# Kernel tuning notes

Hardware: AMD Instinct MI355X
Metric: run time of the kernel (lower is better)

Reference implementation:

```python
import jax, jax.numpy as jnp
import numpy as np

B, T, WARM, H, FIN, MLPW = 8192, 30, 24, 128, 8, 128
WX = ['clouds','pres','precip','temp','rh','ghi','wind_x','wind_y']
TL = ['hour_sin','hour_cos','year_sin','year_cos','elev_angle','azimuth_sin','azimuth_cos']


def setup_inputs() -> dict:
    key = jax.random.key(0)
    ks = jax.random.split(key, 32)
    d = {}
    for i, n in enumerate(WX + TL):
        d[n] = jax.random.normal(ks[i], (B, T), dtype=jnp.float32)
    d['irradiance_in'] = jax.random.uniform(ks[20], (B, WARM), dtype=jnp.float32)
    s = lambda fan: 1.0 / np.sqrt(fan).astype(np.float32)
    # LSTM params (flax OptimizedLSTMCell math: fused input/hidden kernels, one bias), gate order i,f,g,o
    d['Wi'] = jax.random.normal(ks[21], (FIN, 4 * H), dtype=jnp.float32) * s(FIN)
    d['Wh'] = jax.random.normal(ks[22], (H, 4 * H), dtype=jnp.float32) * s(H)
    d['b'] = jnp.zeros((4 * H,), jnp.float32)
    # output head: MLP(depth=2, width=128) with relu, then Dense(1)
    d['W1'] = jax.random.normal(ks[23], (H, MLPW), dtype=jnp.float32) * s(H)
    d['b1'] = jnp.zeros((MLPW,), jnp.float32)
    d['W2'] = jax.random.normal(ks[24], (MLPW, MLPW), dtype=jnp.float32) * s(MLPW)
    d['b2'] = jnp.zeros((MLPW,), jnp.float32)
    d['Wout'] = jax.random.normal(ks[25], (MLPW, 1), dtype=jnp.float32) * s(MLPW)
    d['bout'] = jnp.zeros((1,), jnp.float32)
    return d


def reference(clouds, pres, precip, temp, rh, ghi, wind_x, wind_y,
              hour_sin, hour_cos, year_sin, year_cos, elev_angle, azimuth_sin, azimuth_cos,
              irradiance_in, Wi, Wh, b, W1, b1, W2, b2, Wout, bout):
    # FLAGS.weather=False path: x is the time/location feature stack [B, T, 7].
    # Weather features are accepted (as in the original dict) but unused.
    x = jnp.stack([hour_sin, hour_cos, year_sin, year_cos, elev_angle, azimuth_sin, azimuth_cos], axis=-1)
    warm_in = jnp.concatenate([x[:, :WARM], irradiance_in[..., None]], axis=-1)  # [B, 24, 8]
    auto_in = x[:, WARM:]                                                        # [B, 6, 7]

    def lstm_step(c, h, inp):
        z = inp @ Wi + h @ Wh + b                    # [B, 4H]
        i, f, g, o = jnp.split(z, 4, axis=-1)
        c2 = jax.nn.sigmoid(f) * c + jax.nn.sigmoid(i) * jnp.tanh(g)
        h2 = jax.nn.sigmoid(o) * jnp.tanh(c2)
        return c2, h2

    def out_mlp(h):
        h = jax.nn.relu(h @ W1 + b1)
        h = jax.nn.relu(h @ W2 + b2)
        return h @ Wout + bout                       # [..., 1]

    c0 = jnp.zeros((x.shape[0], H), x.dtype)
    h0 = jnp.zeros((x.shape[0], H), x.dtype)

    # warmup: teacher-forced LSTM over observed irradiance
    def warm_step(carry, xt):
        c, h = carry
        c, h = lstm_step(c, h, xt)
        return (c, h), h
    (c, h), hs = jax.lax.scan(warm_step, (c0, h0), jnp.swapaxes(warm_in, 0, 1))
    preds_warm = out_mlp(jnp.swapaxes(hs, 0, 1))     # [B, 24, 1]
    last_pred = preds_warm[:, -1]                    # [B, 1]

    def auto_step(carry, xt):
        c, h, p = carry
        c, h = lstm_step(c, h, jnp.concatenate([xt, p], axis=-1))
        p = out_mlp(h)
        return (c, h, p), p
    _, preds_auto = jax.lax.scan(auto_step, (c, h, last_pred), jnp.swapaxes(auto_in, 0, 1))
    preds_auto = jnp.swapaxes(preds_auto, 0, 1)      # [B, 6, 1]

    pred = jnp.concatenate([preds_warm, preds_auto], axis=1)  # [B, 30, 1]
    return jnp.squeeze(pred, axis=2)                 # [B, 30]
```

## Files before the change

### kernel.cpp

```cpp
#include <hip/hip_runtime.h>


#define T_STEPS 30
#define WARM_N  24

typedef __attribute__((ext_vector_type(8)))  short short8;
typedef __attribute__((ext_vector_type(4)))  float float4v;

struct FeatPtrs { const float* f[7]; };

__device__ __forceinline__ short f2bf(float f){
  unsigned u = __float_as_uint(f);
  unsigned r = (u + 0x7fffu + ((u >> 16) & 1u)) >> 16;
  return (short)r;
}
__device__ __forceinline__ float bf2f(short h){
  return __uint_as_float(((unsigned)(unsigned short)h) << 16);
}

#if __has_builtin(__builtin_amdgcn_rcpf)
#define RCP(x) __builtin_amdgcn_rcpf(x)
#else
#define RCP(x) (1.0f/(x))
#endif

__device__ __forceinline__ float sigm(float x){ return RCP(1.0f + __expf(-x)); }
__device__ __forceinline__ float tanh_(float x){ return 1.0f - 2.0f*RCP(1.0f + __expf(2.0f*x)); }

__global__ void pack_weights(const float* __restrict__ Wi, const float* __restrict__ Wh,
                             const float* __restrict__ W1, const float* __restrict__ W2,
                             short* __restrict__ ws)
{
  int idx = blockIdx.x * 256 + threadIdx.x;
  if (idx >= 224 * 512) return;
  int f    = idx >> 9;
  int r    = idx & 511;
  int lane = r >> 3, j = r & 7;
  int kk   = ((lane >> 4) << 3) + j;
  int c16  = lane & 15;
  float v = 0.0f;
  if (f < 160){
    int wt = f / 20, rem = f % 20, g = rem / 5, ks = rem % 5;
    int col = g * 128 + wt * 16 + c16;
    if (ks == 0){
      if (kk < 8)        v = Wi[kk * 512 + col];
      else if (kk < 16)  v = Wi[(kk - 8) * 512 + col];
      else               v = 0.0f;
    } else {
      v = Wh[((ks - 1) * 32 + kk) * 512 + col];
    }
  } else {
    int f2 = f - 160;
    const float* W = (f2 < 32) ? W1 : W2;
    int f3 = f2 & 31;
    int wt = f3 >> 2, ks = f3 & 3;
    v = W[(ks * 32 + kk) * 128 + wt * 16 + c16];
  }
  ws[idx] = f2bf(v);
}

__global__ __launch_bounds__(512, 2)
void lstm_mfma(FeatPtrs fp, const float* __restrict__ irr,
               const short* __restrict__ wsb,
               const float* __restrict__ bz, const float* __restrict__ b1,
               const float* __restrict__ b2, const float* __restrict__ Wout,
               const float* __restrict__ bout, float* __restrict__ out)
{
  __shared__ __align__(16) short xp[2][1280];
  __shared__ __align__(16) short hhi[4 * 1280];
  __shared__ __align__(16) short hlo[4 * 1280];
  __shared__ __align__(16) short o1p[4 * 1280];
  __shared__ __align__(16) float o2s[32 * 132];
  __shared__ float WoutS[128];
  __shared__ float pS[32];

  const int t   = threadIdx.x;
  const int l   = t & 63;
  const int w   = t >> 6;
  const int c16 = l & 15;
  const int kq  = l >> 4;
  const int r0  = blockIdx.x * 32;

  short8 Bz[4][5], B1f[4], B2f[4];
  {
    const short8* f8 = (const short8*)wsb;
#pragma unroll
    for (int g = 0; g < 4; ++g)
#pragma unroll
      for (int ks = 0; ks < 5; ++ks)
        Bz[g][ks] = f8[((w * 4 + g) * 5 + ks) * 64 + l];
#pragma unroll
    for (int ks = 0; ks < 4; ++ks) B1f[ks] = f8[(160 + w * 4 + ks) * 64 + l];
#pragma unroll
    for (int ks = 0; ks < 4; ++ks) B2f[ks] = f8[(192 + w * 4 + ks) * 64 + l];
  }
  float bzv[4];
#pragma unroll
  for (int g = 0; g < 4; ++g) bzv[g] = bz[g * 128 + w * 16 + c16];
  const float b1v   = b1[w * 16 + c16];
  const float b2v   = b2[w * 16 + c16];
  const float bout0 = bout[0];
  if (t < 128) WoutS[t] = Wout[t];

  {
    int* p = (int*)xp;
    for (int i = t; i < 1280; i += 512) p[i] = 0;
    p = (int*)hhi;
    for (int i = t; i < 2560; i += 512) p[i] = 0;
    p = (int*)hlo;
    for (int i = t; i < 2560; i += 512) p[i] = 0;
  }

  float cst[8];
#pragma unroll
  for (int i = 0; i < 8; ++i) cst[i] = 0.0f;

  const int aoff = c16 * 40 + kq * 8;
  const int wb   = (w >> 1) * 1280 + (w & 1) * 16 + c16;
  __syncthreads();

  if (t < 256){
    int r = t >> 3, j = t & 7;
    float v = (j < 7) ? fp.f[j][(r0 + r) * T_STEPS] : irr[(r0 + r) * WARM_N];
    int base = (r >> 4) * 640 + (r & 15) * 40 + j;
    short hi = f2bf(v);
    xp[0][base] = hi;
    xp[0][base + 8] = f2bf(v - bf2f(hi));
  }
  __syncthreads();

  for (int i = 0; i < 23; ++i){
    if (t < 256){
      int r = t >> 3, j = t & 7;
      float v = (j < 7) ? fp.f[j][(r0 + r) * T_STEPS + (i + 1)]
                        : irr[(r0 + r) * WARM_N + (i + 1)];
      int base = (r >> 4) * 640 + (r & 15) * 40 + j;
      short hi = f2bf(v);
      short* xb = xp[(i + 1) & 1];
      xb[base] = hi;
      xb[base + 8] = f2bf(v - bf2f(hi));
    }
    float4v acc[4][2];
#pragma unroll
    for (int g = 0; g < 4; ++g)
#pragma unroll
      for (int m = 0; m < 2; ++m)
#pragma unroll
        for (int r = 0; r < 4; ++r) acc[g][m][r] = bzv[g];
    float4v m1[2];
#pragma unroll
    for (int m = 0; m < 2; ++m)
#pragma unroll
      for (int r = 0; r < 4; ++r) m1[m][r] = b1v;
    {
      const short* xb = xp[i & 1];
      short8 a0 = *(const short8*)&xb[aoff];
      short8 a1 = *(const short8*)&xb[640 + aoff];
#pragma unroll
      for (int g = 0; g < 4; ++g){
        acc[g][0] = __builtin_amdgcn_mfma_f32_16x16x32_bf16(a0, Bz[g][0], acc[g][0], 0, 0, 0);
        acc[g][1] = __builtin_amdgcn_mfma_f32_16x16x32_bf16(a1, Bz[g][0], acc[g][1], 0, 0, 0);
      }
    }
#pragma unroll
    for (int ks = 0; ks < 4; ++ks){
      short8 ah0 = *(const short8*)&hhi[ks * 1280 + aoff];
      short8 al0 = *(const short8*)&hlo[ks * 1280 + aoff];
      short8 ah1 = *(const short8*)&hhi[ks * 1280 + 640 + aoff];
      short8 al1 = *(const short8*)&hlo[ks * 1280 + 640 + aoff];
#pragma unroll
      for (int g = 0; g < 4; ++g){
        acc[g][0] = __builtin_amdgcn_mfma_f32_16x16x32_bf16(ah0, Bz[g][1 + ks], acc[g][0], 0, 0, 0);
        acc[g][0] = __builtin_amdgcn_mfma_f32_16x16x32_bf16(al0, Bz[g][1 + ks], acc[g][0], 0, 0, 0);
        acc[g][1] = __builtin_amdgcn_mfma_f32_16x16x32_bf16(ah1, Bz[g][1 + ks], acc[g][1], 0, 0, 0);
        acc[g][1] = __builtin_amdgcn_mfma_f32_16x16x32_bf16(al1, Bz[g][1 + ks], acc[g][1], 0, 0, 0);
      }
      if (i >= 1){
        m1[0] = __builtin_amdgcn_mfma_f32_16x16x32_bf16(ah0, B1f[ks], m1[0], 0, 0, 0);
        m1[0] = __builtin_amdgcn_mfma_f32_16x16x32_bf16(al0, B1f[ks], m1[0], 0, 0, 0);
        m1[1] = __builtin_amdgcn_mfma_f32_16x16x32_bf16(ah1, B1f[ks], m1[1], 0, 0, 0);
        m1[1] = __builtin_amdgcn_mfma_f32_16x16x32_bf16(al1, B1f[ks], m1[1], 0, 0, 0);
      }
    }
    if (i >= 1){
#pragma unroll
      for (int m = 0; m < 2; ++m)
#pragma unroll
        for (int r = 0; r < 4; ++r)
          o1p[wb + m * 640 + (kq * 4 + r) * 40] = f2bf(fmaxf(m1[m][r], 0.0f));
    }
    if (i >= 2 && t < 256){
      int r = t >> 3, jj = t & 7;
      const float* orow = &o2s[r * 132 + jj * 16];
      const float* wrow = &WoutS[jj * 16];
      float s = 0.0f;
#pragma unroll
      for (int q = 0; q < 16; ++q) s += orow[q] * wrow[q];
      s += __shfl_down(s, 4, 8);
      s += __shfl_down(s, 2, 8);
      s += __shfl_down(s, 1, 8);
      if (jj == 0){
        float pv = s + bout0;
        out[(r0 + r) * T_STEPS + (i - 2)] = pv;
        pS[r] = pv;
      }
    }
    __syncthreads();

#pragma unroll
    for (int m = 0; m < 2; ++m)
#pragma unroll
      for (int r = 0; r < 4; ++r){
        float zi = acc[0][m][r], zf = acc[1][m][r], zg = acc[2][m][r], zo = acc[3][m][r];
        float c2 = sigm(zf) * cst[m * 4 + r] + sigm(zi) * tanh_(zg);
        cst[m * 4 + r] = c2;
        float h2 = sigm(zo) * tanh_(c2);
        int addr = wb + m * 640 + (kq * 4 + r) * 40;
        short hi = f2bf(h2);
        hhi[addr] = hi;
        hlo[addr] = f2bf(h2 - bf2f(hi));
      }
    if (i >= 1){
      float4v m2[2];
#pragma unroll
      for (int m = 0; m < 2; ++m)
#pragma unroll
        for (int r = 0; r < 4; ++r) m2[m][r] = b2v;
#pragma unroll
      for (int ks = 0; ks < 4; ++ks){
#pragma unroll
        for (int m = 0; m < 2; ++m){
          short8 a = *(const short8*)&o1p[ks * 1280 + m * 640 + aoff];
          m2[m] = __builtin_amdgcn_mfma_f32_16x16x32_bf16(a, B2f[ks], m2[m], 0, 0, 0);
        }
      }
#pragma unroll
      for (int m = 0; m < 2; ++m)
#pragma unroll
        for (int r = 0; r < 4; ++r)
          o2s[(m * 16 + kq * 4 + r) * 132 + w * 16 + c16] = fmaxf(m2[m][r], 0.0f);
    }
    __syncthreads();
  }

  {
    float4v m1[2];
#pragma unroll
    for (int m = 0; m < 2; ++m)
#pragma unroll
      for (int r = 0; r < 4; ++r) m1[m][r] = b1v;
#pragma unroll
    for (int ks = 0; ks < 4; ++ks){
      short8 ah0 = *(const short8*)&hhi[ks * 1280 + aoff];
      short8 al0 = *(const short8*)&hlo[ks * 1280 + aoff];
      short8 ah1 = *(const short8*)&hhi[ks * 1280 + 640 + aoff];
      short8 al1 = *(const short8*)&hlo[ks * 1280 + 640 + aoff];
      m1[0] = __builtin_amdgcn_mfma_f32_16x16x32_bf16(ah0, B1f[ks], m1[0], 0, 0, 0);
      m1[0] = __builtin_amdgcn_mfma_f32_16x16x32_bf16(al0, B1f[ks], m1[0], 0, 0, 0);
      m1[1] = __builtin_amdgcn_mfma_f32_16x16x32_bf16(ah1, B1f[ks], m1[1], 0, 0, 0);
      m1[1] = __builtin_amdgcn_mfma_f32_16x16x32_bf16(al1, B1f[ks], m1[1], 0, 0, 0);
    }
#pragma unroll
    for (int m = 0; m < 2; ++m)
#pragma unroll
      for (int r = 0; r < 4; ++r)
        o1p[wb + m * 640 + (kq * 4 + r) * 40] = f2bf(fmaxf(m1[m][r], 0.0f));
    if (t < 256){
      int r = t >> 3, jj = t & 7;
      const float* orow = &o2s[r * 132 + jj * 16];
      const float* wrow = &WoutS[jj * 16];
      float s = 0.0f;
#pragma unroll
      for (int q = 0; q < 16; ++q) s += orow[q] * wrow[q];
      s += __shfl_down(s, 4, 8);
      s += __shfl_down(s, 2, 8);
      s += __shfl_down(s, 1, 8);
      if (jj == 0){
        float pv = s + bout0;
        out[(r0 + r) * T_STEPS + 21] = pv;
        pS[r] = pv;
      }
    }
    __syncthreads();
    float4v m2[2];
#pragma unroll
    for (int m = 0; m < 2; ++m)
#pragma unroll
      for (int r = 0; r < 4; ++r) m2[m][r] = b2v;
#pragma unroll
    for (int ks = 0; ks < 4; ++ks){
#pragma unroll
      for (int m = 0; m < 2; ++m){
        short8 a = *(const short8*)&o1p[ks * 1280 + m * 640 + aoff];
        m2[m] = __builtin_amdgcn_mfma_f32_16x16x32_bf16(a, B2f[ks], m2[m], 0, 0, 0);
      }
    }
#pragma unroll
    for (int m = 0; m < 2; ++m)
#pragma unroll
      for (int r = 0; r < 4; ++r)
        o2s[(m * 16 + kq * 4 + r) * 132 + w * 16 + c16] = fmaxf(m2[m][r], 0.0f);
    __syncthreads();
    if (t < 256){
      int r = t >> 3, jj = t & 7;
      const float* orow = &o2s[r * 132 + jj * 16];
      const float* wrow = &WoutS[jj * 16];
      float s = 0.0f;
#pragma unroll
      for (int q = 0; q < 16; ++q) s += orow[q] * wrow[q];
      s += __shfl_down(s, 4, 8);
      s += __shfl_down(s, 2, 8);
      s += __shfl_down(s, 1, 8);
      if (jj == 0){
        float pv = s + bout0;
        out[(r0 + r) * T_STEPS + 22] = pv;
        pS[r] = pv;
      }
    }
    __syncthreads();
  }

  for (int s = 23; s < T_STEPS; ++s){
    if (s > 23){
      if (t < 256){
        int r = t >> 3, j = t & 7;
        float v = (j < 7) ? fp.f[j][(r0 + r) * T_STEPS + s] : pS[r];
        int base = (r >> 4) * 640 + (r & 15) * 40 + j;
        short hi = f2bf(v);
        short* xb = xp[s & 1];
        xb[base] = hi;
        xb[base + 8] = f2bf(v - bf2f(hi));
      }
      __syncthreads();
    }
    float4v acc[4][2];
#pragma unroll
    for (int g = 0; g < 4; ++g)
#pragma unroll
      for (int m = 0; m < 2; ++m)
#pragma unroll
        for (int r = 0; r < 4; ++r) acc[g][m][r] = bzv[g];
    {
      const short* xb = xp[s & 1];
      short8 a0 = *(const short8*)&xb[aoff];
      short8 a1 = *(const short8*)&xb[640 + aoff];
#pragma unroll
      for (int g = 0; g < 4; ++g){
        acc[g][0] = __builtin_amdgcn_mfma_f32_16x16x32_bf16(a0, Bz[g][0], acc[g][0], 0, 0, 0);
        acc[g][1] = __builtin_amdgcn_mfma_f32_16x16x32_bf16(a1, Bz[g][0], acc[g][1], 0, 0, 0);
      }
    }
#pragma unroll
    for (int ks = 0; ks < 4; ++ks){
      short8 ah0 = *(const short8*)&hhi[ks * 1280 + aoff];
      short8 al0 = *(const short8*)&hlo[ks * 1280 + aoff];
      short8 ah1 = *(const short8*)&hhi[ks * 1280 + 640 + aoff];
      short8 al1 = *(const short8*)&hlo[ks * 1280 + 640 + aoff];
#pragma unroll
      for (int g = 0; g < 4; ++g){
        acc[g][0] = __builtin_amdgcn_mfma_f32_16x16x32_bf16(ah0, Bz[g][1 + ks], acc[g][0], 0, 0, 0);
        acc[g][0] = __builtin_amdgcn_mfma_f32_16x16x32_bf16(al0, Bz[g][1 + ks], acc[g][0], 0, 0, 0);
        acc[g][1] = __builtin_amdgcn_mfma_f32_16x16x32_bf16(ah1, Bz[g][1 + ks], acc[g][1], 0, 0, 0);
        acc[g][1] = __builtin_amdgcn_mfma_f32_16x16x32_bf16(al1, Bz[g][1 + ks], acc[g][1], 0, 0, 0);
      }
    }
    __syncthreads();
#pragma unroll
    for (int m = 0; m < 2; ++m)
#pragma unroll
      for (int r = 0; r < 4; ++r){
        float zi = acc[0][m][r], zf = acc[1][m][r], zg = acc[2][m][r], zo = acc[3][m][r];
        float c2 = sigm(zf) * cst[m * 4 + r] + sigm(zi) * tanh_(zg);
        cst[m * 4 + r] = c2;
        float h2 = sigm(zo) * tanh_(c2);
        int addr = wb + m * 640 + (kq * 4 + r) * 40;
        short hi = f2bf(h2);
        hhi[addr] = hi;
        hlo[addr] = f2bf(h2 - bf2f(hi));
      }
    __syncthreads();
    float4v m1[2];
#pragma unroll
    for (int m = 0; m < 2; ++m)
#pragma unroll
      for (int r = 0; r < 4; ++r) m1[m][r] = b1v;
#pragma unroll
    for (int ks = 0; ks < 4; ++ks){
      short8 ah0 = *(const short8*)&hhi[ks * 1280 + aoff];
      short8 al0 = *(const short8*)&hlo[ks * 1280 + aoff];
      short8 ah1 = *(const short8*)&hhi[ks * 1280 + 640 + aoff];
      short8 al1 = *(const short8*)&hlo[ks * 1280 + 640 + aoff];
      m1[0] = __builtin_amdgcn_mfma_f32_16x16x32_bf16(ah0, B1f[ks], m1[0], 0, 0, 0);
      m1[0] = __builtin_amdgcn_mfma_f32_16x16x32_bf16(al0, B1f[ks], m1[0], 0, 0, 0);
      m1[1] = __builtin_amdgcn_mfma_f32_16x16x32_bf16(ah1, B1f[ks], m1[1], 0, 0, 0);
      m1[1] = __builtin_amdgcn_mfma_f32_16x16x32_bf16(al1, B1f[ks], m1[1], 0, 0, 0);
    }
#pragma unroll
    for (int m = 0; m < 2; ++m)
#pragma unroll
      for (int r = 0; r < 4; ++r)
        o1p[wb + m * 640 + (kq * 4 + r) * 40] = f2bf(fmaxf(m1[m][r], 0.0f));
    __syncthreads();
    float4v m2[2];
#pragma unroll
    for (int m = 0; m < 2; ++m)
#pragma unroll
      for (int r = 0; r < 4; ++r) m2[m][r] = b2v;
#pragma unroll
    for (int ks = 0; ks < 4; ++ks){
#pragma unroll
      for (int m = 0; m < 2; ++m){
        short8 a = *(const short8*)&o1p[ks * 1280 + m * 640 + aoff];
        m2[m] = __builtin_amdgcn_mfma_f32_16x16x32_bf16(a, B2f[ks], m2[m], 0, 0, 0);
      }
    }
#pragma unroll
    for (int m = 0; m < 2; ++m)
#pragma unroll
      for (int r = 0; r < 4; ++r)
        o2s[(m * 16 + kq * 4 + r) * 132 + w * 16 + c16] = fmaxf(m2[m][r], 0.0f);
    __syncthreads();
    if (t < 256){
      int r = t >> 3, jj = t & 7;
      const float* orow = &o2s[r * 132 + jj * 16];
      const float* wrow = &WoutS[jj * 16];
      float ssum = 0.0f;
#pragma unroll
      for (int q = 0; q < 16; ++q) ssum += orow[q] * wrow[q];
      ssum += __shfl_down(ssum, 4, 8);
      ssum += __shfl_down(ssum, 2, 8);
      ssum += __shfl_down(ssum, 1, 8);
      if (jj == 0){
        float pv = ssum + bout0;
        out[(r0 + r) * T_STEPS + s] = pv;
        pS[r] = pv;
      }
    }
    __syncthreads();
  }
}

extern "C" void kernel_launch(void* const* d_in, const int* in_sizes, int n_in,
                              void* d_out, int out_size, void* d_ws, size_t ws_size,
                              hipStream_t stream)
{
  (void)in_sizes; (void)n_in; (void)out_size; (void)ws_size;
  FeatPtrs fp;
  for (int j = 0; j < 7; ++j) fp.f[j] = (const float*)d_in[8 + j];
  const float* irr  = (const float*)d_in[15];
  const float* Wi   = (const float*)d_in[16];
  const float* Wh   = (const float*)d_in[17];
  const float* bz   = (const float*)d_in[18];
  const float* W1   = (const float*)d_in[19];
  const float* b1   = (const float*)d_in[20];
  const float* W2   = (const float*)d_in[21];
  const float* b2   = (const float*)d_in[22];
  const float* Wout = (const float*)d_in[23];
  const float* bout = (const float*)d_in[24];

  short* ws = (short*)d_ws;
  pack_weights<<<dim3(448), dim3(256), 0, stream>>>(Wi, Wh, W1, W2, ws);
  lstm_mfma<<<dim3(256), dim3(512), 0, stream>>>(
      fp, irr, ws, bz, b1, b2, Wout, bout, (float*)d_out);
}
```

Baseline: 205.8 us.

## Switch LSTM MFMA to fp16 single-pass and overlap autoregressive head with gate matmul

Replaces the bf16 hi/lo split (two MFMAs per product for hidden state and inputs) with a single fp16 MFMA, roughly halving the tensor-core work and LDS traffic per step. The autoregressive loop is restructured so the gate matmul for step s runs before the previous prediction is known. The fed-back prediction's contribution is then added as a rank-1 fp32 correction using cached Wi row 7, which removes one barrier-serialized stage per step. This trades accuracy, since fp16 has a narrower range and the split compensation is gone, for fewer MFMAs and shorter per-step critical paths.

```diff
diff --git a/kernel.cpp b/kernel.cpp
--- a/kernel.cpp
+++ b/kernel.cpp
@@ -4,19 +4,10 @@
 #define T_STEPS 30
 #define WARM_N  24
 
-typedef __attribute__((ext_vector_type(8)))  short short8;
-typedef __attribute__((ext_vector_type(4)))  float float4v;
+typedef _Float16 h8 __attribute__((ext_vector_type(8)));
+typedef __attribute__((ext_vector_type(4))) float float4v;
 
 struct FeatPtrs { const float* f[7]; };
-
-__device__ __forceinline__ short f2bf(float f){
-  unsigned u = __float_as_uint(f);
-  unsigned r = (u + 0x7fffu + ((u >> 16) & 1u)) >> 16;
-  return (short)r;
-}
-__device__ __forceinline__ float bf2f(short h){
-  return __uint_as_float(((unsigned)(unsigned short)h) << 16);
-}
 
 #if __has_builtin(__builtin_amdgcn_rcpf)
 #define RCP(x) __builtin_amdgcn_rcpf(x)
@@ -29,7 +20,7 @@
 
 __global__ void pack_weights(const float* __restrict__ Wi, const float* __restrict__ Wh,
                              const float* __restrict__ W1, const float* __restrict__ W2,
-                             short* __restrict__ ws)
+                             _Float16* __restrict__ ws)
 {
   int idx = blockIdx.x * 256 + threadIdx.x;
   if (idx >= 224 * 512) return;
@@ -42,13 +33,8 @@
   if (f < 160){
     int wt = f / 20, rem = f % 20, g = rem / 5, ks = rem % 5;
     int col = g * 128 + wt * 16 + c16;
-    if (ks == 0){
-      if (kk < 8)        v = Wi[kk * 512 + col];
-      else if (kk < 16)  v = Wi[(kk - 8) * 512 + col];
-      else               v = 0.0f;
-    } else {
-      v = Wh[((ks - 1) * 32 + kk) * 512 + col];
-    }
+    if (ks == 0) v = (kk < 8) ? Wi[kk * 512 + col] : 0.0f;
+    else         v = Wh[((ks - 1) * 32 + kk) * 512 + col];
   } else {
     int f2 = f - 160;
     const float* W = (f2 < 32) ? W1 : W2;
@@ -56,20 +42,43 @@
     int wt = f3 >> 2, ks = f3 & 3;
     v = W[(ks * 32 + kk) * 128 + wt * 16 + c16];
   }
-  ws[idx] = f2bf(v);
+  ws[idx] = (_Float16)v;
 }
+
+__device__ __forceinline__ void head_do(int t, int r0, int step,
+    const float* o2s, const float* WoutS, float bout0,
+    float* __restrict__ out, float* pS)
+{
+  if (t < 256){
+    int r = t >> 3, jj = t & 7;
+    const float* orow = &o2s[r * 132 + jj * 16];
+    const float* wrow = &WoutS[jj * 16];
+    float s = 0.0f;
+#pragma unroll
+    for (int q = 0; q < 16; ++q) s += orow[q] * wrow[q];
+    s += __shfl_down(s, 4, 8);
+    s += __shfl_down(s, 2, 8);
+    s += __shfl_down(s, 1, 8);
+    if (jj == 0){
+      float pv = s + bout0;
+      out[(r0 + r) * T_STEPS + step] = pv;
+      pS[r] = pv;
+    }
+  }
+}
+
+#define MFMA16 __builtin_amdgcn_mfma_f32_16x16x32_f16
 
 __global__ __launch_bounds__(512, 2)
 void lstm_mfma(FeatPtrs fp, const float* __restrict__ irr,
-               const short* __restrict__ wsb,
+               const _Float16* __restrict__ wsb,
                const float* __restrict__ bz, const float* __restrict__ b1,
                const float* __restrict__ b2, const float* __restrict__ Wout,
                const float* __restrict__ bout, float* __restrict__ out)
 {
-  __shared__ __align__(16) short xp[2][1280];
-  __shared__ __align__(16) short hhi[4 * 1280];
-  __shared__ __align__(16) short hlo[4 * 1280];
-  __shared__ __align__(16) short o1p[4 * 1280];
+  __shared__ __align__(16) _Float16 xp[2][1280];
+  __shared__ __align__(16) _Float16 hp [4 * 1280];
+  __shared__ __align__(16) _Float16 o1p[4 * 1280];
   __shared__ __align__(16) float o2s[32 * 132];
   __shared__ float WoutS[128];
   __shared__ float pS[32];
@@ -81,9 +90,9 @@
   const int kq  = l >> 4;
   const int r0  = blockIdx.x * 32;
 
-  short8 Bz[4][5], B1f[4], B2f[4];
+  h8 Bz[4][5], B1f[4], B2f[4];
   {
-    const short8* f8 = (const short8*)wsb;
+    const h8* f8 = (const h8*)wsb;
 #pragma unroll
     for (int g = 0; g < 4; ++g)
 #pragma unroll
@@ -94,9 +103,12 @@
 #pragma unroll
     for (int ks = 0; ks < 4; ++ks) B2f[ks] = f8[(192 + w * 4 + ks) * 64 + l];
   }
-  float bzv[4];
-#pragma unroll
-  for (int g = 0; g < 4; ++g) bzv[g] = bz[g * 128 + w * 16 + c16];
+  float bzv[4], wi7[4];
+#pragma unroll
+  for (int g = 0; g < 4; ++g){
+    bzv[g] = bz[g * 128 + w * 16 + c16];
+    wi7[g] = (float)wsb[((w * 4 + g) * 5) * 512 + c16 * 8 + 7];
+  }
   const float b1v   = b1[w * 16 + c16];
   const float b2v   = b2[w * 16 + c16];
   const float bout0 = bout[0];
@@ -105,9 +117,7 @@
   {
     int* p = (int*)xp;
     for (int i = t; i < 1280; i += 512) p[i] = 0;
-    p = (int*)hhi;
-    for (int i = t; i < 2560; i += 512) p[i] = 0;
-    p = (int*)hlo;
+    p = (int*)hp;
     for (int i = t; i < 2560; i += 512) p[i] = 0;
   }
 
@@ -122,10 +132,7 @@
   if (t < 256){
     int r = t >> 3, j = t & 7;
     float v = (j < 7) ? fp.f[j][(r0 + r) * T_STEPS] : irr[(r0 + r) * WARM_N];
-    int base = (r >> 4) * 640 + (r & 15) * 40 + j;
-    short hi = f2bf(v);
-    xp[0][base] = hi;
-    xp[0][base + 8] = f2bf(v - bf2f(hi));
+    xp[0][(r >> 4) * 640 + (r & 15) * 40 + j] = (_Float16)v;
   }
   __syncthreads();
 
@@ -134,11 +141,7 @@
       int r = t >> 3, j = t & 7;
       float v = (j < 7) ? fp.f[j][(r0 + r) * T_STEPS + (i + 1)]
                         : irr[(r0 + r) * WARM_N + (i + 1)];
-      int base = (r >> 4) * 640 + (r & 15) * 40 + j;
-      short hi = f2bf(v);
-      short* xb = xp[(i + 1) & 1];
-      xb[base] = hi;
-      xb[base + 8] = f2bf(v - bf2f(hi));
+      xp[(i + 1) & 1][(r >> 4) * 640 + (r & 15) * 40 + j] = (_Float16)v;
     }
     float4v acc[4][2];
 #pragma unroll
@@ -153,33 +156,27 @@
 #pragma unroll
       for (int r = 0; r < 4; ++r) m1[m][r] = b1v;
     {
-      const short* xb = xp[i & 1];
-      short8 a0 = *(const short8*)&xb[aoff];
-      short8 a1 = *(const short8*)&xb[640 + aoff];
+      const _Float16* xb = xp[i & 1];
+      h8 a0 = *(const h8*)&xb[aoff];
+      h8 a1 = *(const h8*)&xb[640 + aoff];
 #pragma unroll
       for (int g = 0; g < 4; ++g){
-        acc[g][0] = __builtin_amdgcn_mfma_f32_16x16x32_bf16(a0, Bz[g][0], acc[g][0], 0, 0, 0);
-        acc[g][1] = __builtin_amdgcn_mfma_f32_16x16x32_bf16(a1, Bz[g][0], acc[g][1], 0, 0, 0);
+        acc[g][0] = MFMA16(a0, Bz[g][0], acc[g][0], 0, 0, 0);
+        acc[g][1] = MFMA16(a1, Bz[g][0], acc[g][1], 0, 0, 0);
       }
     }
 #pragma unroll
     for (int ks = 0; ks < 4; ++ks){
-      short8 ah0 = *(const short8*)&hhi[ks * 1280 + aoff];
-      short8 al0 = *(const short8*)&hlo[ks * 1280 + aoff];
-      short8 ah1 = *(const short8*)&hhi[ks * 1280 + 640 + aoff];
-      short8 al1 = *(const short8*)&hlo[ks * 1280 + 640 + aoff];
+      h8 ah0 = *(const h8*)&hp[ks * 1280 + aoff];
+      h8 ah1 = *(const h8*)&hp[ks * 1280 + 640 + aoff];
 #pragma unroll
       for (int g = 0; g < 4; ++g){
-        acc[g][0] = __builtin_amdgcn_mfma_f32_16x16x32_bf16(ah0, Bz[g][1 + ks], acc[g][0], 0, 0, 0);
-        acc[g][0] = __builtin_amdgcn_mfma_f32_16x16x32_bf16(al0, Bz[g][1 + ks], acc[g][0], 0, 0, 0);
-        acc[g][1] = __builtin_amdgcn_mfma_f32_16x16x32_bf16(ah1, Bz[g][1 + ks], acc[g][1], 0, 0, 0);
-        acc[g][1] = __builtin_amdgcn_mfma_f32_16x16x32_bf16(al1, Bz[g][1 + ks], acc[g][1], 0, 0, 0);
+        acc[g][0] = MFMA16(ah0, Bz[g][1 + ks], acc[g][0], 0, 0, 0);
+        acc[g][1] = MFMA16(ah1, Bz[g][1 + ks], acc[g][1], 0, 0, 0);
       }
       if (i >= 1){
-        m1[0] = __builtin_amdgcn_mfma_f32_16x16x32_bf16(ah0, B1f[ks], m1[0], 0, 0, 0);
-        m1[0] = __builtin_amdgcn_mfma_f32_16x16x32_bf16(al0, B1f[ks], m1[0], 0, 0, 0);
-        m1[1] = __builtin_amdgcn_mfma_f32_16x16x32_bf16(ah1, B1f[ks], m1[1], 0, 0, 0);
-        m1[1] = __builtin_amdgcn_mfma_f32_16x16x32_bf16(al1, B1f[ks], m1[1], 0, 0, 0);
+        m1[0] = MFMA16(ah0, B1f[ks], m1[0], 0, 0, 0);
+        m1[1] = MFMA16(ah1, B1f[ks], m1[1], 0, 0, 0);
       }
     }
     if (i >= 1){
@@ -187,24 +184,9 @@
       for (int m = 0; m < 2; ++m)
 #pragma unroll
         for (int r = 0; r < 4; ++r)
-          o1p[wb + m * 640 + (kq * 4 + r) * 40] = f2bf(fmaxf(m1[m][r], 0.0f));
-    }
-    if (i >= 2 && t < 256){
-      int r = t >> 3, jj = t & 7;
-      const float* orow = &o2s[r * 132 + jj * 16];
-      const float* wrow = &WoutS[jj * 16];
-      float s = 0.0f;
-#pragma unroll
-      for (int q = 0; q < 16; ++q) s += orow[q] * wrow[q];
-      s += __shfl_down(s, 4, 8);
-      s += __shfl_down(s, 2, 8);
-      s += __shfl_down(s, 1, 8);
-      if (jj == 0){
-        float pv = s + bout0;
-        out[(r0 + r) * T_STEPS + (i - 2)] = pv;
-        pS[r] = pv;
-      }
-    }
+          o1p[wb + m * 640 + (kq * 4 + r) * 40] = (_Float16)fmaxf(m1[m][r], 0.0f);
+    }
+    if (i >= 2) head_do(t, r0, i - 2, o2s, WoutS, bout0, out, pS);
     __syncthreads();
 
 #pragma unroll
@@ -215,10 +197,7 @@
         float c2 = sigm(zf) * cst[m * 4 + r] + sigm(zi) * tanh_(zg);
         cst[m * 4 + r] = c2;
         float h2 = sigm(zo) * tanh_(c2);
-        int addr = wb + m * 640 + (kq * 4 + r) * 40;
-        short hi = f2bf(h2);
-        hhi[addr] = hi;
-        hlo[addr] = f2bf(h2 - bf2f(hi));
+        hp[wb + m * 640 + (kq * 4 + r) * 40] = (_Float16)h2;
       }
     if (i >= 1){
       float4v m2[2];
@@ -228,11 +207,10 @@
         for (int r = 0; r < 4; ++r) m2[m][r] = b2v;
 #pragma unroll
       for (int ks = 0; ks < 4; ++ks){
-#pragma unroll
-        for (int m = 0; m < 2; ++m){
-          short8 a = *(const short8*)&o1p[ks * 1280 + m * 640 + aoff];
-          m2[m] = __builtin_amdgcn_mfma_f32_16x16x32_bf16(a, B2f[ks], m2[m], 0, 0, 0);
-        }
+        h8 a0 = *(const h8*)&o1p[ks * 1280 + aoff];
+        h8 a1 = *(const h8*)&o1p[ks * 1280 + 640 + aoff];
+        m2[0] = MFMA16(a0, B2f[ks], m2[0], 0, 0, 0);
+        m2[1] = MFMA16(a1, B2f[ks], m2[1], 0, 0, 0);
       }
 #pragma unroll
       for (int m = 0; m < 2; ++m)
@@ -243,128 +221,90 @@
     __syncthreads();
   }
 
-  {
+  head_do(t, r0, 21, o2s, WoutS, bout0, out, pS);
+  __syncthreads();
+
+  for (int s = 23; s < T_STEPS; ++s){
+    if (s < T_STEPS - 1 && t < 256){
+      int r = t >> 3, j = t & 7;
+      float v = (j < 7) ? fp.f[j][(r0 + r) * T_STEPS + (s + 1)] : 0.0f;
+      xp[(s + 1) & 1][(r >> 4) * 640 + (r & 15) * 40 + j] = (_Float16)v;
+    }
+    float4v acc[4][2];
+#pragma unroll
+    for (int g = 0; g < 4; ++g)
+#pragma unroll
+      for (int m = 0; m < 2; ++m)
+#pragma unroll
+        for (int r = 0; r < 4; ++r) acc[g][m][r] = bzv[g];
     float4v m1[2];
 #pragma unroll
     for (int m = 0; m < 2; ++m)
 #pragma unroll
       for (int r = 0; r < 4; ++r) m1[m][r] = b1v;
+    {
+      const _Float16* xb = xp[s & 1];
+      h8 a0 = *(const h8*)&xb[aoff];
+      h8 a1 = *(const h8*)&xb[640 + aoff];
+#pragma unroll
+      for (int g = 0; g < 4; ++g){
+        acc[g][0] = MFMA16(a0, Bz[g][0], acc[g][0], 0, 0, 0);
+        acc[g][1] = MFMA16(a1, Bz[g][0], acc[g][1], 0, 0, 0);
+      }
+    }
 #pragma unroll
     for (int ks = 0; ks < 4; ++ks){
-      short8 ah0 = *(const short8*)&hhi[ks * 1280 + aoff];
-      short8 al0 = *(const short8*)&hlo[ks * 1280 + aoff];
-      short8 ah1 = *(const short8*)&hhi[ks * 1280 + 640 + aoff];
-      short8 al1 = *(const short8*)&hlo[ks * 1280 + 640 + aoff];
-      m1[0] = __builtin_amdgcn_mfma_f32_16x16x32_bf16(ah0, B1f[ks], m1[0], 0, 0, 0);
-      m1[0] = __builtin_amdgcn_mfma_f32_16x16x32_bf16(al0, B1f[ks], m1[0], 0, 0, 0);
-      m1[1] = __builtin_amdgcn_mfma_f32_16x16x32_bf16(ah1, B1f[ks], m1[1], 0, 0, 0);
-      m1[1] = __builtin_amdgcn_mfma_f32_16x16x32_bf16(al1, B1f[ks], m1[1], 0, 0, 0);
+      h8 ah0 = *(const h8*)&hp[ks * 1280 + aoff];
+      h8 ah1 = *(const h8*)&hp[ks * 1280 + 640 + aoff];
+#pragma unroll
+      for (int g = 0; g < 4; ++g){
+        acc[g][0] = MFMA16(ah0, Bz[g][1 + ks], acc[g][0], 0, 0, 0);
+        acc[g][1] = MFMA16(ah1, Bz[g][1 + ks], acc[g][1], 0, 0, 0);
+      }
+      m1[0] = MFMA16(ah0, B1f[ks], m1[0], 0, 0, 0);
+      m1[1] = MFMA16(ah1, B1f[ks], m1[1], 0, 0, 0);
     }
 #pragma unroll
     for (int m = 0; m < 2; ++m)
 #pragma unroll
       for (int r = 0; r < 4; ++r)
-        o1p[wb + m * 640 + (kq * 4 + r) * 40] = f2bf(fmaxf(m1[m][r], 0.0f));
-    if (t < 256){
-      int r = t >> 3, jj = t & 7;
-      const float* orow = &o2s[r * 132 + jj * 16];
-      const float* wrow = &WoutS[jj * 16];
-      float s = 0.0f;
-#pragma unroll
-      for (int q = 0; q < 16; ++q) s += orow[q] * wrow[q];
-      s += __shfl_down(s, 4, 8);
-      s += __shfl_down(s, 2, 8);
-      s += __shfl_down(s, 1, 8);
-      if (jj == 0){
-        float pv = s + bout0;
-        out[(r0 + r) * T_STEPS + 21] = pv;
-        pS[r] = pv;
-      }
-    }
-    __syncthreads();
-    float4v m2[2];
-#pragma unroll
-    for (int m = 0; m < 2; ++m)
-#pragma unroll
-      for (int r = 0; r < 4; ++r) m2[m][r] = b2v;
-#pragma unroll
-    for (int ks = 0; ks < 4; ++ks){
-#pragma unroll
-      for (int m = 0; m < 2; ++m){
-        short8 a = *(const short8*)&o1p[ks * 1280 + m * 640 + aoff];
-        m2[m] = __builtin_amdgcn_mfma_f32_16x16x32_bf16(a, B2f[ks], m2[m], 0, 0, 0);
-      }
-    }
-#pragma unroll
-    for (int m = 0; m < 2; ++m)
-#pragma unroll
-      for (int r = 0; r < 4; ++r)
-        o2s[(m * 16 + kq * 4 + r) * 132 + w * 16 + c16] = fmaxf(m2[m][r], 0.0f);
-    __syncthreads();
-    if (t < 256){
-      int r = t >> 3, jj = t & 7;
-      const float* orow = &o2s[r * 132 + jj * 16];
-      const float* wrow = &WoutS[jj * 16];
-      float s = 0.0f;
-#pragma unroll
-      for (int q = 0; q < 16; ++q) s += orow[q] * wrow[q];
-      s += __shfl_down(s, 4, 8);
-      s += __shfl_down(s, 2, 8);
-      s += __shfl_down(s, 1, 8);
-      if (jj == 0){
-        float pv = s + bout0;
-        out[(r0 + r) * T_STEPS + 22] = pv;
-        pS[r] = pv;
-      }
-    }
-    __syncthreads();
-  }
-
-  for (int s = 23; s < T_STEPS; ++s){
-    if (s > 23){
-      if (t < 256){
-        int r = t >> 3, j = t & 7;
-        float v = (j < 7) ? fp.f[j][(r0 + r) * T_STEPS + s] : pS[r];
-        int base = (r >> 4) * 640 + (r & 15) * 40 + j;
-        short hi = f2bf(v);
-        short* xb = xp[s & 1];
-        xb[base] = hi;
-        xb[base + 8] = f2bf(v - bf2f(hi));
-      }
-      __syncthreads();
-    }
-    float4v acc[4][2];
-#pragma unroll
-    for (int g = 0; g < 4; ++g)
-#pragma unroll
-      for (int m = 0; m < 2; ++m)
-#pragma unroll
-        for (int r = 0; r < 4; ++r) acc[g][m][r] = bzv[g];
+        o1p[wb + m * 640 + (kq * 4 + r) * 40] = (_Float16)fmaxf(m1[m][r], 0.0f);
+    __syncthreads();
+
     {
-      const short* xb = xp[s & 1];
-      short8 a0 = *(const short8*)&xb[aoff];
-      short8 a1 = *(const short8*)&xb[640 + aoff];
-#pragma unroll
-      for (int g = 0; g < 4; ++g){
-        acc[g][0] = __builtin_amdgcn_mfma_f32_16x16x32_bf16(a0, Bz[g][0], acc[g][0], 0, 0, 0);
-        acc[g][1] = __builtin_amdgcn_mfma_f32_16x16x32_bf16(a1, Bz[g][0], acc[g][1], 0, 0, 0);
-      }
-    }
-#pragma unroll
-    for (int ks = 0; ks < 4; ++ks){
-      short8 ah0 = *(const short8*)&hhi[ks * 1280 + aoff];
-      short8 al0 = *(const short8*)&hlo[ks * 1280 + aoff];
-      short8 ah1 = *(const short8*)&hhi[ks * 1280 + 640 + aoff];
-      short8 al1 = *(const short8*)&hlo[ks * 1280 + 640 + aoff];
-#pragma unroll
-      for (int g = 0; g < 4; ++g){
-        acc[g][0] = __builtin_amdgcn_mfma_f32_16x16x32_bf16(ah0, Bz[g][1 + ks], acc[g][0], 0, 0, 0);
-        acc[g][0] = __builtin_amdgcn_mfma_f32_16x16x32_bf16(al0, Bz[g][1 + ks], acc[g][0], 0, 0, 0);
-        acc[g][1] = __builtin_amdgcn_mfma_f32_16x16x32_bf16(ah1, Bz[g][1 + ks], acc[g][1], 0, 0, 0);
-        acc[g][1] = __builtin_amdgcn_mfma_f32_16x16x32_bf16(al1, Bz[g][1 + ks], acc[g][1], 0, 0, 0);
-      }
-    }
-    __syncthreads();
+      float4v m2[2];
+#pragma unroll
+      for (int m = 0; m < 2; ++m)
+#pragma unroll
+        for (int r = 0; r < 4; ++r) m2[m][r] = b2v;
+#pragma unroll
+      for (int ks = 0; ks < 4; ++ks){
+        h8 a0 = *(const h8*)&o1p[ks * 1280 + aoff];
+        h8 a1 = *(const h8*)&o1p[ks * 1280 + 640 + aoff];
+        m2[0] = MFMA16(a0, B2f[ks], m2[0], 0, 0, 0);
+        m2[1] = MFMA16(a1, B2f[ks], m2[1], 0, 0, 0);
+      }
+#pragma unroll
+      for (int m = 0; m < 2; ++m)
+#pragma unroll
+        for (int r = 0; r < 4; ++r)
+          o2s[(m * 16 + kq * 4 + r) * 132 + w * 16 + c16] = fmaxf(m2[m][r], 0.0f);
+    }
+    __syncthreads();
+
+    head_do(t, r0, s - 1, o2s, WoutS, bout0, out, pS);
+    __syncthreads();
+
+    if (s >= 24){
+#pragma unroll
+      for (int m = 0; m < 2; ++m)
+#pragma unroll
+        for (int r = 0; r < 4; ++r){
+          float pv = pS[m * 16 + kq * 4 + r];
+#pragma unroll
+          for (int g = 0; g < 4; ++g) acc[g][m][r] += pv * wi7[g];
+        }
+    }
 #pragma unroll
     for (int m = 0; m < 2; ++m)
 #pragma unroll
@@ -373,12 +313,12 @@
         float c2 = sigm(zf) * cst[m * 4 + r] + sigm(zi) * tanh_(zg);
         cst[m * 4 + r] = c2;
         float h2 = sigm(zo) * tanh_(c2);
-        int addr = wb + m * 640 + (kq * 4 + r) * 40;
-        short hi = f2bf(h2);
-        hhi[addr] = hi;
-        hlo[addr] = f2bf(h2 - bf2f(hi));
-      }
-    __syncthreads();
+        hp[wb + m * 640 + (kq * 4 + r) * 40] = (_Float16)h2;
+      }
+    __syncthreads();
+  }
+
+  {
     float4v m1[2];
 #pragma unroll
     for (int m = 0; m < 2; ++m)
@@ -386,20 +326,16 @@
       for (int r = 0; r < 4; ++r) m1[m][r] = b1v;
 #pragma unroll
     for (int ks = 0; ks < 4; ++ks){
-      short8 ah0 = *(const short8*)&hhi[ks * 1280 + aoff];
-      short8 al0 = *(const short8*)&hlo[ks * 1280 + aoff];
-      short8 ah1 = *(const short8*)&hhi[ks * 1280 + 640 + aoff];
-      short8 al1 = *(const short8*)&hlo[ks * 1280 + 640 + aoff];
-      m1[0] = __builtin_amdgcn_mfma_f32_16x16x32_bf16(ah0, B1f[ks], m1[0], 0, 0, 0);
-      m1[0] = __builtin_amdgcn_mfma_f32_16x16x32_bf16(al0, B1f[ks], m1[0], 0, 0, 0);
-      m1[1] = __builtin_amdgcn_mfma_f32_16x16x32_bf16(ah1, B1f[ks], m1[1], 0, 0, 0);
-      m1[1] = __builtin_amdgcn_mfma_f32_16x16x32_bf16(al1, B1f[ks], m1[1], 0, 0, 0);
+      h8 ah0 = *(const h8*)&hp[ks * 1280 + aoff];
+      h8 ah1 = *(const h8*)&hp[ks * 1280 + 640 + aoff];
+      m1[0] = MFMA16(ah0, B1f[ks], m1[0], 0, 0, 0);
+      m1[1] = MFMA16(ah1, B1f[ks], m1[1], 0, 0, 0);
     }
 #pragma unroll
     for (int m = 0; m < 2; ++m)
 #pragma unroll
       for (int r = 0; r < 4; ++r)
-        o1p[wb + m * 640 + (kq * 4 + r) * 40] = f2bf(fmaxf(m1[m][r], 0.0f));
+        o1p[wb + m * 640 + (kq * 4 + r) * 40] = (_Float16)fmaxf(m1[m][r], 0.0f);
     __syncthreads();
     float4v m2[2];
 #pragma unroll
@@ -408,11 +344,10 @@
       for (int r = 0; r < 4; ++r) m2[m][r] = b2v;
 #pragma unroll
     for (int ks = 0; ks < 4; ++ks){
-#pragma unroll
-      for (int m = 0; m < 2; ++m){
-        short8 a = *(const short8*)&o1p[ks * 1280 + m * 640 + aoff];
-        m2[m] = __builtin_amdgcn_mfma_f32_16x16x32_bf16(a, B2f[ks], m2[m], 0, 0, 0);
-      }
+      h8 a0 = *(const h8*)&o1p[ks * 1280 + aoff];
+      h8 a1 = *(const h8*)&o1p[ks * 1280 + 640 + aoff];
+      m2[0] = MFMA16(a0, B2f[ks], m2[0], 0, 0, 0);
+      m2[1] = MFMA16(a1, B2f[ks], m2[1], 0, 0, 0);
     }
 #pragma unroll
     for (int m = 0; m < 2; ++m)
@@ -420,23 +355,7 @@
       for (int r = 0; r < 4; ++r)
         o2s[(m * 16 + kq * 4 + r) * 132 + w * 16 + c16] = fmaxf(m2[m][r], 0.0f);
     __syncthreads();
-    if (t < 256){
-      int r = t >> 3, jj = t & 7;
-      const float* orow = &o2s[r * 132 + jj * 16];
-      const float* wrow = &WoutS[jj * 16];
-      float ssum = 0.0f;
-#pragma unroll
-      for (int q = 0; q < 16; ++q) ssum += orow[q] * wrow[q];
-      ssum += __shfl_down(ssum, 4, 8);
-      ssum += __shfl_down(ssum, 2, 8);
-      ssum += __shfl_down(ssum, 1, 8);
-      if (jj == 0){
-        float pv = ssum + bout0;
-        out[(r0 + r) * T_STEPS + s] = pv;
-        pS[r] = pv;
-      }
-    }
-    __syncthreads();
+    head_do(t, r0, 29, o2s, WoutS, bout0, out, pS);
   }
 }
 
@@ -458,7 +377,7 @@
   const float* Wout = (const float*)d_in[23];
   const float* bout = (const float*)d_in[24];
 
-  short* ws = (short*)d_ws;
+  _Float16* ws = (_Float16*)d_ws;
   pack_weights<<<dim3(448), dim3(256), 0, stream>>>(Wi, Wh, W1, W2, ws);
   lstm_mfma<<<dim3(256), dim3(512), 0, stream>>>(
       fp, irr, ws, bz, b1, b2, Wout, bout, (float*)d_out);
```

Result: faster. 182.3 us (-11.4%).
